# Performance work log

Measured on AMD Instinct MI355X. Metric: run time of the kernel, lower is better.

The kernel has to match this reference:

```python
import jax, jax.numpy as jnp
import numpy as np

NUM_POINTS = 32
POINT_DIM = 4
HIDDEN_DIM = 256
BATCH = 8192


def setup_inputs() -> dict:
    key = jax.random.key(0)
    k1, k2, k3 = jax.random.split(key, 3)
    path_data = jax.random.normal(k1, (BATCH, NUM_POINTS * POINT_DIM), dtype=jnp.float32)
    # per-step Linear(point_dim+hidden_dim -> hidden_dim); torch Linear weight layout [out, in]
    fan_in = POINT_DIM + HIDDEN_DIM
    scale = 1.0 / np.sqrt(fan_in)
    W = jax.random.uniform(k2, (NUM_POINTS, HIDDEN_DIM, fan_in), dtype=jnp.float32, minval=-scale, maxval=scale)
    b = jax.random.uniform(k3, (NUM_POINTS, HIDDEN_DIM), dtype=jnp.float32, minval=-scale, maxval=scale)
    return {"path_data": path_data, "W": W, "b": b}


def reference(path_data, W, b):
    P, H = W.shape[0], W.shape[1]
    B = path_data.shape[0]
    pd = W.shape[2] - H
    # chunks: [P, B, point_dim]
    chunks = path_data.reshape(B, P, pd).transpose(1, 0, 2)

    def step(h, xs):
        wp, Wi, bi = xs
        # concat order matches torch: (curr_hidden, current_wp)
        combined = jnp.concatenate([h, wp], axis=1)  # [B, H+pd]
        h_new = jax.nn.relu(combined @ Wi.T + bi)    # [B, H]
        return h_new, h_new

    h0 = jnp.zeros((B, H), dtype=path_data.dtype)
    _, feats = jax.lax.scan(step, h0, (chunks, W, b))  # feats: [P, B, H]
    return feats.transpose(1, 0, 2).reshape(B, P * H)
```

## Files before the change

kernel.cpp:

```cpp
#include <hip/hip_runtime.h>

typedef __attribute__((ext_vector_type(8))) short bf16x8;
typedef __attribute__((ext_vector_type(16))) float f32x16;
typedef __attribute__((ext_vector_type(4))) float f32x4;

#define NPTS 32
#define HID 256
#define FANIN 260
#define NKB 17
#define OUTSTRIDE 8192

__device__ __forceinline__ unsigned short f2bf(float f) {
  unsigned u = __builtin_bit_cast(unsigned, f);
  u += 0x7fffu + ((u >> 16) & 1u);
  return (unsigned short)(u >> 16);
}

__global__ __launch_bounds__(256) void prep_kernel(
    const float* __restrict__ W, const float* __restrict__ bias,
    bf16x8* __restrict__ pack) {
  __shared__ float wl[32 * FANIN];
  const int p = blockIdx.x >> 3;
  const int nb = blockIdx.x & 7;
  const int t = threadIdx.x;
  const f32x4* src = reinterpret_cast<const f32x4*>(
      W + ((size_t)p * HID + nb * 32) * FANIN);
  for (int i = t; i < 32 * FANIN / 4; i += 256)
    *reinterpret_cast<f32x4*>(wl + i * 4) = src[i];
  __syncthreads();
  const int lane = t & 63;
  const int wv = t >> 6;
  const int m = lane & 31;
  const int g = lane >> 5;
  const float* rowp = wl + m * FANIN;
  for (int kb = wv; kb < NKB; kb += 4) {
    unsigned short e[8];
#pragma unroll
    for (int i = 0; i < 8; ++i) e[i] = 0;
    if (kb < 16) {
      int k0 = kb * 16 + g * 8;
#pragma unroll
      for (int i = 0; i < 8; ++i) e[i] = f2bf(rowp[k0 + i]);
    } else if (g == 0) {
      e[0] = f2bf(rowp[256]);
      e[1] = f2bf(rowp[257]);
      e[2] = f2bf(rowp[258]);
      e[3] = f2bf(rowp[259]);
      e[4] = f2bf(bias[p * HID + nb * 32 + m]);
    }
    bf16x8 v;
#pragma unroll
    for (int i = 0; i < 8; ++i) v[i] = (short)e[i];
    pack[(((size_t)p * 8 + nb) * NKB + kb) * 64 + lane] = v;
  }
}

__global__ __launch_bounds__(512, 2) void enc_kernel(
    const float* __restrict__ path, const bf16x8* __restrict__ pack,
    float* __restrict__ out) {
  __shared__ __align__(16) char lds[98304];
  const int tid = threadIdx.x;
  const int lane = tid & 63;
  const int w = tid >> 6;
  const int col = lane & 31;
  const int g = lane >> 5;
  const int b0 = blockIdx.x * 32;
  const int swz = col << 4;

  {
    f32x4 z = {0.0f, 0.0f, 0.0f, 0.0f};
    *reinterpret_cast<f32x4*>(lds + tid * 32) = z;
    *reinterpret_cast<f32x4*>(lds + tid * 32 + 16) = z;
  }

  const float4* prow =
      reinterpret_cast<const float4*>(path + (size_t)(b0 + col) * 128);
  float* outbase = out + (size_t)b0 * OUTSTRIDE;

  bf16x8 BC[NKB];
  {
    const bf16x8* Bp0 = pack + (size_t)w * NKB * 64 + lane;
#pragma unroll
    for (int kb = 0; kb < NKB; ++kb) BC[kb] = Bp0[kb * 64];
  }
  float4 px = prow[0];
  __syncthreads();

  for (int p = 0; p < NPTS; ++p) {
    const int pn = (p + 1 < NPTS) ? p + 1 : 0;
    const bf16x8* Bnp = pack + ((size_t)(pn * 8 + w) * NKB) * 64 + lane;
    f32x16 acc0, acc1;
#pragma unroll
    for (int i = 0; i < 16; ++i) {
      acc0[i] = 0.0f;
      acc1[i] = 0.0f;
    }
    const char* hb = lds + (p & 1) * 16384;
#pragma unroll
    for (int kb = 0; kb < 16; ++kb) {
      bf16x8 a = *reinterpret_cast<const bf16x8*>(
          hb + col * 512 + ((kb * 32 + g * 16) ^ swz));
      if (kb & 1)
        acc1 = __builtin_amdgcn_mfma_f32_32x32x16_bf16(a, BC[kb], acc1, 0, 0, 0);
      else
        acc0 = __builtin_amdgcn_mfma_f32_32x32x16_bf16(a, BC[kb], acc0, 0, 0, 0);
      BC[kb] = Bnp[kb * 64];
    }
    bf16x8 ax;
#pragma unroll
    for (int i = 0; i < 8; ++i) ax[i] = 0;
    if (g == 0) {
      ax[0] = (short)f2bf(px.x);
      ax[1] = (short)f2bf(px.y);
      ax[2] = (short)f2bf(px.z);
      ax[3] = (short)f2bf(px.w);
      ax[4] = (short)0x3F80;
    }
    acc0 = __builtin_amdgcn_mfma_f32_32x32x16_bf16(ax, BC[16], acc0, 0, 0, 0);
    BC[16] = Bnp[16 * 64];
    px = prow[pn];

    char* hn = lds + ((p + 1) & 1) * 16384;
    float* st = reinterpret_cast<float*>(lds + 32768 + (p & 1) * 32768);
#pragma unroll
    for (int r = 0; r < 16; ++r) {
      int rr = (r & 3) + 8 * (r >> 2) + 4 * g;
      float v = fmaxf(acc0[r] + acc1[r], 0.0f);
      st[rr * 256 + w * 32 + col] = v;
      *reinterpret_cast<unsigned short*>(
          hn + rr * 512 + (((w * 32 + col) * 2) ^ (rr << 4))) = f2bf(v);
    }
    asm volatile("s_waitcnt lgkmcnt(0)" ::: "memory");
    __builtin_amdgcn_s_barrier();

    const f32x4* stf =
        reinterpret_cast<const f32x4*>(lds + 32768 + (p & 1) * 32768);
    float* ob = outbase + p * 256;
#pragma unroll
    for (int s = 0; s < 4; ++s) {
      int i = s * 512 + tid;
      f32x4 v = stf[i];
      int r = i >> 6;
      int c = (i & 63) << 2;
      __builtin_nontemporal_store(
          v, reinterpret_cast<f32x4*>(ob + (size_t)r * OUTSTRIDE + c));
    }
  }
}

extern "C" void kernel_launch(void* const* d_in, const int* in_sizes, int n_in,
                              void* d_out, int out_size, void* d_ws,
                              size_t ws_size, hipStream_t stream) {
  const float* path = (const float*)d_in[0];
  const float* W = (const float*)d_in[1];
  const float* bias = (const float*)d_in[2];
  float* out = (float*)d_out;
  bf16x8* pack = (bf16x8*)d_ws;

  prep_kernel<<<256, 256, 0, stream>>>(W, bias, pack);
  enc_kernel<<<256, 512, 0, stream>>>(path, pack, out);
}
```

Baseline: 97.69 us.

## Store outputs directly from registers, batch LDS A loads, raise MFMA priority

The fp32 staging buffer in LDS is removed. Each lane now writes its relu outputs straight to global memory as scalar nontemporal stores, which drops the LDS store/load round trip and cuts LDS from 96KB to 32KB. All 16 A-fragments are loaded from LDS before the MFMA chain, and the chain is wrapped in s_setprio to favour matrix issue. The trade-off is that the global writes become 4-byte scattered stores (32 consecutive floats per row per wave) instead of 16-byte coalesced vectors, and holding the A fragments in registers raises register pressure.

```diff
diff --git a/kernel.cpp b/kernel.cpp
--- a/kernel.cpp
+++ b/kernel.cpp
@@ -58,7 +58,7 @@
 __global__ __launch_bounds__(512, 2) void enc_kernel(
     const float* __restrict__ path, const bf16x8* __restrict__ pack,
     float* __restrict__ out) {
-  __shared__ __align__(16) char lds[98304];
+  __shared__ __align__(16) char lds[32768];
   const int tid = threadIdx.x;
   const int lane = tid & 63;
   const int w = tid >> 6;
@@ -75,7 +75,7 @@
 
   const float4* prow =
       reinterpret_cast<const float4*>(path + (size_t)(b0 + col) * 128);
-  float* outbase = out + (size_t)b0 * OUTSTRIDE;
+  float* outbase = out + (size_t)b0 * OUTSTRIDE + w * 32 + col;
 
   bf16x8 BC[NKB];
   {
@@ -89,23 +89,14 @@
   for (int p = 0; p < NPTS; ++p) {
     const int pn = (p + 1 < NPTS) ? p + 1 : 0;
     const bf16x8* Bnp = pack + ((size_t)(pn * 8 + w) * NKB) * 64 + lane;
-    f32x16 acc0, acc1;
+    const char* hb = lds + (p & 1) * 16384;
+
+    bf16x8 a[16];
 #pragma unroll
-    for (int i = 0; i < 16; ++i) {
-      acc0[i] = 0.0f;
-      acc1[i] = 0.0f;
-    }
-    const char* hb = lds + (p & 1) * 16384;
-#pragma unroll
-    for (int kb = 0; kb < 16; ++kb) {
-      bf16x8 a = *reinterpret_cast<const bf16x8*>(
+    for (int kb = 0; kb < 16; ++kb)
+      a[kb] = *reinterpret_cast<const bf16x8*>(
           hb + col * 512 + ((kb * 32 + g * 16) ^ swz));
-      if (kb & 1)
-        acc1 = __builtin_amdgcn_mfma_f32_32x32x16_bf16(a, BC[kb], acc1, 0, 0, 0);
-      else
-        acc0 = __builtin_amdgcn_mfma_f32_32x32x16_bf16(a, BC[kb], acc0, 0, 0, 0);
-      BC[kb] = Bnp[kb * 64];
-    }
+
     bf16x8 ax;
 #pragma unroll
     for (int i = 0; i < 8; ++i) ax[i] = 0;
@@ -116,35 +107,46 @@
       ax[3] = (short)f2bf(px.w);
       ax[4] = (short)0x3F80;
     }
+
+    f32x16 acc0, acc1;
+#pragma unroll
+    for (int i = 0; i < 16; ++i) {
+      acc0[i] = 0.0f;
+      acc1[i] = 0.0f;
+    }
+
+    __builtin_amdgcn_s_setprio(1);
+#pragma unroll
+    for (int kb = 0; kb < 16; ++kb) {
+      if (kb & 1)
+        acc1 = __builtin_amdgcn_mfma_f32_32x32x16_bf16(a[kb], BC[kb], acc1, 0, 0, 0);
+      else
+        acc0 = __builtin_amdgcn_mfma_f32_32x32x16_bf16(a[kb], BC[kb], acc0, 0, 0, 0);
+      BC[kb] = Bnp[kb * 64];
+    }
     acc0 = __builtin_amdgcn_mfma_f32_32x32x16_bf16(ax, BC[16], acc0, 0, 0, 0);
+    __builtin_amdgcn_s_setprio(0);
     BC[16] = Bnp[16 * 64];
     px = prow[pn];
 
     char* hn = lds + ((p + 1) & 1) * 16384;
-    float* st = reinterpret_cast<float*>(lds + 32768 + (p & 1) * 32768);
+    float vr[16];
 #pragma unroll
     for (int r = 0; r < 16; ++r) {
       int rr = (r & 3) + 8 * (r >> 2) + 4 * g;
       float v = fmaxf(acc0[r] + acc1[r], 0.0f);
-      st[rr * 256 + w * 32 + col] = v;
+      vr[r] = v;
       *reinterpret_cast<unsigned short*>(
           hn + rr * 512 + (((w * 32 + col) * 2) ^ (rr << 4))) = f2bf(v);
     }
+    float* outp = outbase + p * 256;
+#pragma unroll
+    for (int r = 0; r < 16; ++r) {
+      int rr = (r & 3) + 8 * (r >> 2) + 4 * g;
+      __builtin_nontemporal_store(vr[r], outp + (size_t)rr * OUTSTRIDE);
+    }
     asm volatile("s_waitcnt lgkmcnt(0)" ::: "memory");
     __builtin_amdgcn_s_barrier();
-
-    const f32x4* stf =
-        reinterpret_cast<const f32x4*>(lds + 32768 + (p & 1) * 32768);
-    float* ob = outbase + p * 256;
-#pragma unroll
-    for (int s = 0; s < 4; ++s) {
-      int i = s * 512 + tid;
-      f32x4 v = stf[i];
-      int r = i >> 6;
-      int c = (i & 63) << 2;
-      __builtin_nontemporal_store(
-          v, reinterpret_cast<f32x4*>(ob + (size_t)r * OUTSTRIDE + c));
-    }
   }
 }
 
```

Measured after the change: 115.0 us. 17.7% more time.
